# Performance work log

Measured on AMD Instinct MI355X. Metric: run time of the kernel, lower is better.

The kernel has to match this reference:

```python
import jax, jax.numpy as jnp
import numpy as np

B, N, M, D, F, H = 8, 512, 512, 512, 512, 8
D_H, F_H = D // H, F // H


def setup_inputs() -> dict:
    key = jax.random.key(0)
    ks = jax.random.split(key, 7)
    X = jax.random.normal(ks[0], (B, N, D), dtype=jnp.float32)
    V = jax.random.normal(ks[1], (B, M, F), dtype=jnp.float32)
    # learned parameters, init normal(0, 0.02) as in the torch module
    W_Q_1 = 0.02 * jax.random.normal(ks[2], (H, N, D_H, D_H), dtype=jnp.float32)
    W_Q_2 = 0.02 * jax.random.normal(ks[3], (H, N, M, D_H), dtype=jnp.float32)
    W_V = 0.02 * jax.random.normal(ks[4], (H, F_H, F_H), dtype=jnp.float32)
    O_w = 0.02 * jax.random.normal(ks[5], (F, F), dtype=jnp.float32)
    O_b = jnp.zeros((F,), dtype=jnp.float32)
    return {"X": X, "V": V, "W_Q_1": W_Q_1, "W_Q_2": W_Q_2,
            "W_V": W_V, "O_w": O_w, "O_b": O_b}


def reference(X, V, W_Q_1, W_Q_2, W_V, O_w, O_b):
    b, n, d = X.shape
    _, m, f = V.shape
    Xh = X.reshape(b, n, H, d // H)      # [B,N,H,D_H]
    Vh = V.reshape(b, m, H, f // H)      # [B,M,H,F_H]
    # 'hndd' repeats d within one operand -> diagonal of W_Q_1's last two dims
    # (faithful to torch.einsum semantics): per-position per-channel scale.
    Q_1 = jnp.einsum('bnhd,hndd->bhnd', Xh, W_Q_1)
    Q_1 = jax.nn.gelu(Q_1, approximate=False)  # torch nn.GELU default = exact erf
    Q_2 = jnp.einsum('bhnd,hnmd->bhnm', Q_1, W_Q_2)  # synthesized attention logits
    A = jax.nn.softmax(Q_2, axis=3)                  # softmax over M
    # 'hff' likewise takes the diagonal of W_V -> per-head channel scale fused
    # with the attention-weighted value aggregation.
    Y = jnp.einsum('bhnm,bmhf,hff->bnhf', A, Vh, W_V)
    Y = Y.reshape(b, n, f)
    return Y @ O_w.T + O_b
```

## Files before the change

### kernel.cpp

```cpp
#include <hip/hip_runtime.h>
#include <cstdint>

#define B_ 8
#define N_ 512
#define M_ 512
#define D_ 512
#define F_ 512
#define H_ 8
#define DH_ 64
#define FH_ 64

typedef __attribute__((ext_vector_type(8))) short bf16x8;
typedef __attribute__((ext_vector_type(4))) float f32x4;

__device__ __forceinline__ unsigned short f2bf(float x) {
    unsigned u = __float_as_uint(x);
    return (unsigned short)((u + 0x7fffu + ((u >> 16) & 1u)) >> 16);
}
__device__ __forceinline__ float bf2f(unsigned short b) {
    return __uint_as_float(((unsigned)b) << 16);
}

template <int CTRL>
__device__ __forceinline__ float dpp_add(float x) {
    int y = __builtin_amdgcn_update_dpp(0, __float_as_int(x), CTRL, 0xf, 0xf, true);
    return x + __int_as_float(y);
}

__global__ __launch_bounds__(256, 4) void syn_k_attn(const float* __restrict__ X,
                                                     const float* __restrict__ W1,
                                                     const float* __restrict__ W2,
                                                     float* __restrict__ A) {
    int hn = blockIdx.x;
    int h = hn >> 9, n = hn & 511;
    int t = threadIdx.x;
    int wave = t >> 6, lane = t & 63;
    __shared__ float q1s[8 * 68];
    __shared__ float logits[8 * 520];

    {
        int d = t & 63;
        int b0 = t >> 6;
        float w = W1[(size_t)hn * (DH_ * DH_) + d * (DH_ + 1)];
        #pragma unroll
        for (int i = 0; i < 2; ++i) {
            int bi = b0 + i * 4;
            float x = X[((size_t)(bi * N_ + n)) * D_ + h * DH_ + d];
            float v = x * w;
            q1s[bi * 68 + d] = 0.5f * v * (1.0f + erff(v * 0.70710678118654752440f));
        }
    }
    __syncthreads();

    int mr = lane >> 3, c = lane & 7;
    float4 qa[8], qb[8];
    #pragma unroll
    for (int b = 0; b < 8; ++b) {
        qa[b] = *(const float4*)&q1s[b * 68 + c * 8];
        qb[b] = *(const float4*)&q1s[b * 68 + c * 8 + 4];
    }

    const float* w2 = W2 + (size_t)hn * ((size_t)M_ * DH_);
    #pragma unroll 4
    for (int g = 0; g < 16; ++g) {
        int m = (wave + g * 4) * 8 + mr;
        const float* wr = w2 + (size_t)m * DH_ + c * 8;
        float4 wa = *(const float4*)wr;
        float4 wb = *(const float4*)(wr + 4);
        float acc[8];
        #pragma unroll
        for (int b = 0; b < 8; ++b) {
            float a0 = wa.x * qa[b].x + wa.y * qa[b].y + wa.z * qa[b].z + wa.w * qa[b].w
                     + wb.x * qb[b].x + wb.y * qb[b].y + wb.z * qb[b].z + wb.w * qb[b].w;
            a0 = dpp_add<0xB1>(a0);
            a0 = dpp_add<0x4E>(a0);
            a0 = dpp_add<0x124>(a0);
            acc[b] = a0;
        }
        float lo = c == 0 ? acc[0] : c == 1 ? acc[1] : c == 2 ? acc[2] : acc[3];
        float hi = c == 0 ? acc[4] : c == 1 ? acc[5] : c == 2 ? acc[6] : acc[7];
        if (c < 4) {
            logits[c * 520 + m] = lo;
            logits[(c + 4) * 520 + m] = hi;
        }
    }
    __syncthreads();

    for (int bb = wave; bb < 8; bb += 4) {
        const float* lrow = &logits[bb * 520 + lane * 8];
        float4 va = *(const float4*)lrow;
        float4 vb = *(const float4*)(lrow + 4);
        float v[8] = {va.x, va.y, va.z, va.w, vb.x, vb.y, vb.z, vb.w};
        float mx = v[0];
        #pragma unroll
        for (int i = 1; i < 8; ++i) mx = fmaxf(mx, v[i]);
        #pragma unroll
        for (int s = 1; s < 64; s <<= 1) mx = fmaxf(mx, __shfl_xor(mx, s));
        float e[8]; float sum = 0.f;
        #pragma unroll
        for (int i = 0; i < 8; ++i) { e[i] = expf(v[i] - mx); sum += e[i]; }
        #pragma unroll
        for (int s = 1; s < 64; s <<= 1) sum += __shfl_xor(sum, s);
        float inv = 1.0f / sum;
        float* outp = A + ((size_t)(bb * H_ + h) * N_ + n) * M_ + lane * 8;
        float4 o0 = make_float4(e[0] * inv, e[1] * inv, e[2] * inv, e[3] * inv);
        float4 o1 = make_float4(e[4] * inv, e[5] * inv, e[6] * inv, e[7] * inv);
        *(float4*)outp = o0;
        *(float4*)(outp + 4) = o1;
    }
}

__global__ __launch_bounds__(256) void syn_k_pv(const float* __restrict__ A,
                                                const float* __restrict__ V,
                                                const float* __restrict__ WV,
                                                unsigned short* __restrict__ Yhi,
                                                unsigned short* __restrict__ Ylo) {
    int bh = blockIdx.y;
    int b = bh >> 3, h = bh & 7;
    int n0 = blockIdx.x * 64;
    int t = threadIdx.x;
    int tx = t & 15, ty = t >> 4;
    __shared__ float Alds[64 * 64];
    __shared__ float Vlds[64 * 64];
    float acc[4][4] = {};
    const float* Abase = A + ((size_t)bh * N_ + n0) * M_;
    const float* Vbase = V + (size_t)b * ((size_t)M_ * F_) + h * FH_;
    int kk = tx * 4;
    for (int m0 = 0; m0 < M_; m0 += 64) {
        #pragma unroll
        for (int it = 0; it < 4; ++it) {
            int r = ty + it * 16;
            float4 a4 = *(const float4*)(Abase + (size_t)r * M_ + m0 + kk);
            int slot = ((r >> 2) ^ tx) & 15;
            float* p = &Alds[kk * 64 + slot * 4 + (r & 3)];
            p[0] = a4.x; p[64] = a4.y; p[128] = a4.z; p[192] = a4.w;
            float4 v4 = *(const float4*)(Vbase + (size_t)(m0 + r) * F_ + kk);
            *(float4*)&Vlds[r * 64 + kk] = v4;
        }
        __syncthreads();
        #pragma unroll 2
        for (int k4 = 0; k4 < 16; ++k4) {
            int sa = ((ty ^ k4) & 15) * 4;
            #pragma unroll
            for (int kj = 0; kj < 4; ++kj) {
                int k = k4 * 4 + kj;
                float4 a4 = *(const float4*)&Alds[k * 64 + sa];
                float4 v4 = *(const float4*)&Vlds[k * 64 + tx * 4];
                float ar[4] = {a4.x, a4.y, a4.z, a4.w};
                float vr[4] = {v4.x, v4.y, v4.z, v4.w};
                #pragma unroll
                for (int i = 0; i < 4; ++i)
                    #pragma unroll
                    for (int j = 0; j < 4; ++j)
                        acc[i][j] += ar[i] * vr[j];
            }
        }
        __syncthreads();
    }
    float s_[4];
    #pragma unroll
    for (int j = 0; j < 4; ++j)
        s_[j] = WV[(size_t)h * (FH_ * FH_) + (tx * 4 + j) * (FH_ + 1)];
    #pragma unroll
    for (int i = 0; i < 4; ++i) {
        int row = n0 + ty * 4 + i;
        float ys[4];
        #pragma unroll
        for (int j = 0; j < 4; ++j) ys[j] = acc[i][j] * s_[j];
        unsigned short hb[4], lb[4];
        #pragma unroll
        for (int j = 0; j < 4; ++j) {
            hb[j] = f2bf(ys[j]);
            lb[j] = f2bf(ys[j] - bf2f(hb[j]));
        }
        size_t base = ((size_t)(b * N_ + row)) * F_ + h * FH_ + tx * 4;
        uint2 hv, lv;
        hv.x = (unsigned)hb[0] | ((unsigned)hb[1] << 16);
        hv.y = (unsigned)hb[2] | ((unsigned)hb[3] << 16);
        lv.x = (unsigned)lb[0] | ((unsigned)lb[1] << 16);
        lv.y = (unsigned)lb[2] | ((unsigned)lb[3] << 16);
        *(uint2*)(Yhi + base) = hv;
        *(uint2*)(Ylo + base) = lv;
    }
}

__global__ __launch_bounds__(256) void syn_k_splitw(const float* __restrict__ Ow,
                                                    unsigned short* __restrict__ Whi,
                                                    unsigned short* __restrict__ Wlo) {
    int i = (blockIdx.x * 256 + threadIdx.x) * 4;
    float4 v = *(const float4*)(Ow + i);
    float vv[4] = {v.x, v.y, v.z, v.w};
    unsigned short hb[4], lb[4];
    #pragma unroll
    for (int j = 0; j < 4; ++j) {
        hb[j] = f2bf(vv[j]);
        lb[j] = f2bf(vv[j] - bf2f(hb[j]));
    }
    uint2 hv, lv;
    hv.x = (unsigned)hb[0] | ((unsigned)hb[1] << 16);
    hv.y = (unsigned)hb[2] | ((unsigned)hb[3] << 16);
    lv.x = (unsigned)lb[0] | ((unsigned)lb[1] << 16);
    lv.y = (unsigned)lb[2] | ((unsigned)lb[3] << 16);
    *(uint2*)(Whi + i) = hv;
    *(uint2*)(Wlo + i) = lv;
}

__global__ __launch_bounds__(256) void syn_k_out_mfma(const unsigned short* __restrict__ Yhi,
                                                      const unsigned short* __restrict__ Ylo,
                                                      const unsigned short* __restrict__ Whi,
                                                      const unsigned short* __restrict__ Wlo,
                                                      const float* __restrict__ Ob,
                                                      float* __restrict__ out) {
    int r0 = blockIdx.x * 64;
    int f0 = blockIdx.y * 64;
    int t = threadIdx.x;
    int lane = t & 63, wave = t >> 6;
    int wr = wave >> 1, wc = wave & 1;
    __shared__ __align__(16) unsigned short Al[64 * 64];
    __shared__ __align__(16) unsigned short Bl[64 * 64];
    f32x4 acc[2][2];
    #pragma unroll
    for (int i = 0; i < 2; ++i)
        #pragma unroll
        for (int j = 0; j < 2; ++j)
            acc[i][j] = (f32x4){0.f, 0.f, 0.f, 0.f};

    const unsigned short* Aseg[3] = {Yhi, Yhi, Ylo};
    const unsigned short* Bseg[3] = {Whi, Wlo, Whi};

    int srow = t >> 3, skg = t & 7;
    int sslot = skg ^ (srow & 7);
    unsigned aoff0 = srow * 64 + sslot * 8;
    unsigned aoff1 = (srow + 32) * 64 + sslot * 8;

    for (int seg = 0; seg < 3; ++seg) {
        const unsigned short* Ag0 = Aseg[seg] + (size_t)(r0 + srow) * 512 + skg * 8;
        const unsigned short* Ag1 = Aseg[seg] + (size_t)(r0 + srow + 32) * 512 + skg * 8;
        const unsigned short* Bg0 = Bseg[seg] + (size_t)(f0 + srow) * 512 + skg * 8;
        const unsigned short* Bg1 = Bseg[seg] + (size_t)(f0 + srow + 32) * 512 + skg * 8;
        #pragma unroll 1
        for (int kb = 0; kb < 512; kb += 64) {
            float4 a0 = *(const float4*)(Ag0 + kb);
            float4 a1 = *(const float4*)(Ag1 + kb);
            float4 b0 = *(const float4*)(Bg0 + kb);
            float4 b1 = *(const float4*)(Bg1 + kb);
            *(float4*)&Al[aoff0] = a0;
            *(float4*)&Al[aoff1] = a1;
            *(float4*)&Bl[aoff0] = b0;
            *(float4*)&Bl[aoff1] = b1;
            __syncthreads();
            #pragma unroll
            for (int m = 0; m < 2; ++m) {
                int kslot = (m * 4 + (lane >> 4)) ^ (lane & 7);
                bf16x8 af[2], bfr[2];
                #pragma unroll
                for (int q = 0; q < 2; ++q) {
                    int arow = wr * 32 + q * 16 + (lane & 15);
                    af[q] = *(const bf16x8*)&Al[arow * 64 + kslot * 8];
                    int brow = wc * 32 + q * 16 + (lane & 15);
                    bfr[q] = *(const bf16x8*)&Bl[brow * 64 + kslot * 8];
                }
                #pragma unroll
                for (int i = 0; i < 2; ++i)
                    #pragma unroll
                    for (int j = 0; j < 2; ++j)
                        acc[i][j] = __builtin_amdgcn_mfma_f32_16x16x32_bf16(
                            af[i], bfr[j], acc[i][j], 0, 0, 0);
            }
            __syncthreads();
        }
    }

    int crow = r0 + wr * 32 + (lane >> 4) * 4;
    int ccol = f0 + wc * 32 + (lane & 15);
    float ob0 = Ob[ccol], ob1 = Ob[ccol + 16];
    #pragma unroll
    for (int i = 0; i < 2; ++i)
        #pragma unroll
        for (int j = 0; j < 2; ++j) {
            float obv = (j == 0) ? ob0 : ob1;
            #pragma unroll
            for (int r = 0; r < 4; ++r) {
                int row = crow + i * 16 + r;
                out[(size_t)row * F_ + ccol + j * 16] = acc[i][j][r] + obv;
            }
        }
}

extern "C" void kernel_launch(void* const* d_in, const int* in_sizes, int n_in,
                              void* d_out, int out_size, void* d_ws, size_t ws_size,
                              hipStream_t stream) {
    const float* X  = (const float*)d_in[0];
    const float* V  = (const float*)d_in[1];
    const float* W1 = (const float*)d_in[2];
    const float* W2 = (const float*)d_in[3];
    const float* WV = (const float*)d_in[4];
    const float* Ow = (const float*)d_in[5];
    const float* Ob = (const float*)d_in[6];
    float* out = (float*)d_out;

    float* ws = (float*)d_ws;
    float* A = ws;
    unsigned short* Yhi = (unsigned short*)(A + (size_t)B_ * H_ * N_ * M_);
    unsigned short* Ylo = Yhi + (size_t)B_ * N_ * F_;
    unsigned short* Whi = Ylo + (size_t)B_ * N_ * F_;
    unsigned short* Wlo = Whi + (size_t)F_ * F_;

    syn_k_splitw<<<(F_ * F_) / (256 * 4), 256, 0, stream>>>(Ow, Whi, Wlo);
    syn_k_attn<<<H_ * N_, 256, 0, stream>>>(X, W1, W2, A);
    syn_k_pv<<<dim3(N_ / 64, B_ * H_), 256, 0, stream>>>(A, V, WV, Yhi, Ylo);
    syn_k_out_mfma<<<dim3((B_ * N_) / 64, F_ / 64), 256, 0, stream>>>(Yhi, Ylo, Whi, Wlo, Ob, out);
}
```

Measured before the change: 200.4 us.

## Move attention-value product to split-bf16 MFMA and fuse out-proj segments

Replaces the scalar FP32 A·V kernel with an MFMA kernel that splits A (on the fly) and V (via a new pre-transpose kernel into workspace) into bf16 hi/lo parts and runs three MFMAs per tile to emulate FP32 accuracy. The output projection is also restructured to load hi and lo tiles together in one pass instead of three sequential segments, which cuts global reloads of Yhi and Whi. The intent is to move the heavy A·V FLOPs off the vector ALUs onto matrix cores. In exchange it adds a V transpose/split launch, more LDS per block, and a small precision loss from dropping the lo·lo term.

```diff
diff --git a/kernel.cpp b/kernel.cpp
--- a/kernel.cpp
+++ b/kernel.cpp
@@ -12,6 +12,7 @@
 
 typedef __attribute__((ext_vector_type(8))) short bf16x8;
 typedef __attribute__((ext_vector_type(4))) float f32x4;
+typedef __attribute__((ext_vector_type(8))) unsigned short u16x8;
 
 __device__ __forceinline__ unsigned short f2bf(float x) {
     unsigned u = __float_as_uint(x);
@@ -110,80 +111,6 @@
     }
 }
 
-__global__ __launch_bounds__(256) void syn_k_pv(const float* __restrict__ A,
-                                                const float* __restrict__ V,
-                                                const float* __restrict__ WV,
-                                                unsigned short* __restrict__ Yhi,
-                                                unsigned short* __restrict__ Ylo) {
-    int bh = blockIdx.y;
-    int b = bh >> 3, h = bh & 7;
-    int n0 = blockIdx.x * 64;
-    int t = threadIdx.x;
-    int tx = t & 15, ty = t >> 4;
-    __shared__ float Alds[64 * 64];
-    __shared__ float Vlds[64 * 64];
-    float acc[4][4] = {};
-    const float* Abase = A + ((size_t)bh * N_ + n0) * M_;
-    const float* Vbase = V + (size_t)b * ((size_t)M_ * F_) + h * FH_;
-    int kk = tx * 4;
-    for (int m0 = 0; m0 < M_; m0 += 64) {
-        #pragma unroll
-        for (int it = 0; it < 4; ++it) {
-            int r = ty + it * 16;
-            float4 a4 = *(const float4*)(Abase + (size_t)r * M_ + m0 + kk);
-            int slot = ((r >> 2) ^ tx) & 15;
-            float* p = &Alds[kk * 64 + slot * 4 + (r & 3)];
-            p[0] = a4.x; p[64] = a4.y; p[128] = a4.z; p[192] = a4.w;
-            float4 v4 = *(const float4*)(Vbase + (size_t)(m0 + r) * F_ + kk);
-            *(float4*)&Vlds[r * 64 + kk] = v4;
-        }
-        __syncthreads();
-        #pragma unroll 2
-        for (int k4 = 0; k4 < 16; ++k4) {
-            int sa = ((ty ^ k4) & 15) * 4;
-            #pragma unroll
-            for (int kj = 0; kj < 4; ++kj) {
-                int k = k4 * 4 + kj;
-                float4 a4 = *(const float4*)&Alds[k * 64 + sa];
-                float4 v4 = *(const float4*)&Vlds[k * 64 + tx * 4];
-                float ar[4] = {a4.x, a4.y, a4.z, a4.w};
-                float vr[4] = {v4.x, v4.y, v4.z, v4.w};
-                #pragma unroll
-                for (int i = 0; i < 4; ++i)
-                    #pragma unroll
-                    for (int j = 0; j < 4; ++j)
-                        acc[i][j] += ar[i] * vr[j];
-            }
-        }
-        __syncthreads();
-    }
-    float s_[4];
-    #pragma unroll
-    for (int j = 0; j < 4; ++j)
-        s_[j] = WV[(size_t)h * (FH_ * FH_) + (tx * 4 + j) * (FH_ + 1)];
-    #pragma unroll
-    for (int i = 0; i < 4; ++i) {
-        int row = n0 + ty * 4 + i;
-        float ys[4];
-        #pragma unroll
-        for (int j = 0; j < 4; ++j) ys[j] = acc[i][j] * s_[j];
-        unsigned short hb[4], lb[4];
-        #pragma unroll
-        for (int j = 0; j < 4; ++j) {
-            hb[j] = f2bf(ys[j]);
-            lb[j] = f2bf(ys[j] - bf2f(hb[j]));
-        }
-        size_t base = ((size_t)(b * N_ + row)) * F_ + h * FH_ + tx * 4;
-        uint2 hv, lv;
-        hv.x = (unsigned)hb[0] | ((unsigned)hb[1] << 16);
-        hv.y = (unsigned)hb[2] | ((unsigned)hb[3] << 16);
-        lv.x = (unsigned)lb[0] | ((unsigned)lb[1] << 16);
-        lv.y = (unsigned)lb[2] | ((unsigned)lb[3] << 16);
-        *(uint2*)(Yhi + base) = hv;
-        *(uint2*)(Ylo + base) = lv;
-    }
-}
-
 __global__ __launch_bounds__(256) void syn_k_splitw(const float* __restrict__ Ow,
                                                     unsigned short* __restrict__ Whi,
                                                     unsigned short* __restrict__ Wlo) {
@@ -203,6 +130,133 @@
     lv.y = (unsigned)lb[2] | ((unsigned)lb[3] << 16);
     *(uint2*)(Whi + i) = hv;
     *(uint2*)(Wlo + i) = lv;
+}
+
+__global__ __launch_bounds__(256) void syn_k_splitv(const float* __restrict__ V,
+                                                    unsigned short* __restrict__ Vthi,
+                                                    unsigned short* __restrict__ Vtlo) {
+    int bh = blockIdx.x;
+    int b = bh >> 3, h = bh & 7;
+    int t = threadIdx.x;
+    __shared__ float lds[64 * 68];
+    for (int m0 = 0; m0 < M_; m0 += 64) {
+        int m = t >> 2, fo = (t & 3) * 16;
+        const float* src = V + ((size_t)(b * M_ + m0 + m)) * F_ + h * FH_ + fo;
+        #pragma unroll
+        for (int i = 0; i < 4; ++i)
+            *(float4*)&lds[m * 68 + fo + i * 4] = *(const float4*)(src + i * 4);
+        __syncthreads();
+        int f = t >> 2, mo = (t & 3) * 16;
+        unsigned short hb[16], lb[16];
+        #pragma unroll
+        for (int i = 0; i < 16; ++i) {
+            float x = lds[(mo + i) * 68 + f];
+            hb[i] = f2bf(x);
+            lb[i] = f2bf(x - bf2f(hb[i]));
+        }
+        size_t base = ((size_t)(bh * 64 + f)) * 512 + m0 + mo;
+        *(u16x8*)(Vthi + base) = *(u16x8*)hb;
+        *(u16x8*)(Vthi + base + 8) = *(u16x8*)&hb[8];
+        *(u16x8*)(Vtlo + base) = *(u16x8*)lb;
+        *(u16x8*)(Vtlo + base + 8) = *(u16x8*)&lb[8];
+        __syncthreads();
+    }
+}
+
+__global__ __launch_bounds__(256) void syn_k_pv_mfma(const float* __restrict__ A,
+                                                     const unsigned short* __restrict__ Vthi,
+                                                     const unsigned short* __restrict__ Vtlo,
+                                                     const float* __restrict__ WV,
+                                                     unsigned short* __restrict__ Yhi,
+                                                     unsigned short* __restrict__ Ylo) {
+    int bh = blockIdx.y;
+    int b = bh >> 3, h = bh & 7;
+    int n0 = blockIdx.x * 64;
+    int t = threadIdx.x;
+    int lane = t & 63, wave = t >> 6;
+    int wr = wave >> 1, wc = wave & 1;
+    __shared__ __align__(16) unsigned short Alh[64 * 64], All[64 * 64];
+    __shared__ __align__(16) unsigned short Blh[64 * 64], Bll[64 * 64];
+    f32x4 acc[2][2];
+    #pragma unroll
+    for (int i = 0; i < 2; ++i)
+        #pragma unroll
+        for (int j = 0; j < 2; ++j) acc[i][j] = (f32x4){0.f, 0.f, 0.f, 0.f};
+
+    int srow = t >> 3, skg = t & 7;
+    int sslot = skg ^ (srow & 7);
+    const float* Abase = A + ((size_t)bh * N_ + n0) * M_;
+    const unsigned short* Vhb = Vthi + ((size_t)bh * 64) * 512;
+    const unsigned short* Vlb = Vtlo + ((size_t)bh * 64) * 512;
+
+    #pragma unroll 1
+    for (int mb = 0; mb < 8; ++mb) {
+        int m0 = mb * 64;
+        #pragma unroll
+        for (int rr = 0; rr < 2; ++rr) {
+            int row = srow + rr * 32;
+            const float* ap = Abase + (size_t)row * M_ + m0 + skg * 8;
+            float4 x0 = *(const float4*)ap;
+            float4 x1 = *(const float4*)(ap + 4);
+            float xs[8] = {x0.x, x0.y, x0.z, x0.w, x1.x, x1.y, x1.z, x1.w};
+            unsigned short hb[8], lb[8];
+            #pragma unroll
+            for (int i = 0; i < 8; ++i) {
+                hb[i] = f2bf(xs[i]);
+                lb[i] = f2bf(xs[i] - bf2f(hb[i]));
+            }
+            *(u16x8*)&Alh[row * 64 + sslot * 8] = *(u16x8*)hb;
+            *(u16x8*)&All[row * 64 + sslot * 8] = *(u16x8*)lb;
+            *(u16x8*)&Blh[row * 64 + sslot * 8] =
+                *(const u16x8*)(Vhb + (size_t)row * 512 + m0 + skg * 8);
+            *(u16x8*)&Bll[row * 64 + sslot * 8] =
+                *(const u16x8*)(Vlb + (size_t)row * 512 + m0 + skg * 8);
+        }
+        __syncthreads();
+        #pragma unroll
+        for (int mg = 0; mg < 2; ++mg) {
+            int kslot = (mg * 4 + (lane >> 4)) ^ (lane & 7);
+            bf16x8 afh[2], afl[2], bfh[2], bfl[2];
+            #pragma unroll
+            for (int q = 0; q < 2; ++q) {
+                int arow = wr * 32 + q * 16 + (lane & 15);
+                afh[q] = *(const bf16x8*)&Alh[arow * 64 + kslot * 8];
+                afl[q] = *(const bf16x8*)&All[arow * 64 + kslot * 8];
+                int brow = wc * 32 + q * 16 + (lane & 15);
+                bfh[q] = *(const bf16x8*)&Blh[brow * 64 + kslot * 8];
+                bfl[q] = *(const bf16x8*)&Bll[brow * 64 + kslot * 8];
+            }
+            #pragma unroll
+            for (int i = 0; i < 2; ++i)
+                #pragma unroll
+                for (int j = 0; j < 2; ++j) {
+                    acc[i][j] = __builtin_amdgcn_mfma_f32_16x16x32_bf16(afh[i], bfh[j], acc[i][j], 0, 0, 0);
+                    acc[i][j] = __builtin_amdgcn_mfma_f32_16x16x32_bf16(afh[i], bfl[j], acc[i][j], 0, 0, 0);
+                    acc[i][j] = __builtin_amdgcn_mfma_f32_16x16x32_bf16(afl[i], bfh[j], acc[i][j], 0, 0, 0);
+                }
+        }
+        __syncthreads();
+    }
+
+    int crow = n0 + wr * 32 + (lane >> 4) * 4;
+    int ccol = wc * 32 + (lane & 15);
+    #pragma unroll
+    for (int j = 0; j < 2; ++j) {
+        int f = ccol + j * 16;
+        float s = WV[(size_t)h * (FH_ * FH_) + f * (FH_ + 1)];
+        #pragma unroll
+        for (int i = 0; i < 2; ++i)
+            #pragma unroll
+            for (int r = 0; r < 4; ++r) {
+                int row = crow + i * 16 + r;
+                float y = acc[i][j][r] * s;
+                unsigned short hb = f2bf(y);
+                unsigned short lb = f2bf(y - bf2f(hb));
+                size_t base = ((size_t)(b * N_ + row)) * F_ + h * FH_ + f;
+                Yhi[base] = hb;
+                Ylo[base] = lb;
+            }
+    }
 }
 
 __global__ __launch_bounds__(256) void syn_k_out_mfma(const unsigned short* __restrict__ Yhi,
@@ -216,59 +270,53 @@
     int t = threadIdx.x;
     int lane = t & 63, wave = t >> 6;
     int wr = wave >> 1, wc = wave & 1;
-    __shared__ __align__(16) unsigned short Al[64 * 64];
-    __shared__ __align__(16) unsigned short Bl[64 * 64];
+    __shared__ __align__(16) unsigned short Alh[64 * 64], All[64 * 64];
+    __shared__ __align__(16) unsigned short Blh[64 * 64], Bll[64 * 64];
     f32x4 acc[2][2];
     #pragma unroll
     for (int i = 0; i < 2; ++i)
         #pragma unroll
-        for (int j = 0; j < 2; ++j)
-            acc[i][j] = (f32x4){0.f, 0.f, 0.f, 0.f};
-
-    const unsigned short* Aseg[3] = {Yhi, Yhi, Ylo};
-    const unsigned short* Bseg[3] = {Whi, Wlo, Whi};
+        for (int j = 0; j < 2; ++j) acc[i][j] = (f32x4){0.f, 0.f, 0.f, 0.f};
 
     int srow = t >> 3, skg = t & 7;
     int sslot = skg ^ (srow & 7);
-    unsigned aoff0 = srow * 64 + sslot * 8;
-    unsigned aoff1 = (srow + 32) * 64 + sslot * 8;
-
-    for (int seg = 0; seg < 3; ++seg) {
-        const unsigned short* Ag0 = Aseg[seg] + (size_t)(r0 + srow) * 512 + skg * 8;
-        const unsigned short* Ag1 = Aseg[seg] + (size_t)(r0 + srow + 32) * 512 + skg * 8;
-        const unsigned short* Bg0 = Bseg[seg] + (size_t)(f0 + srow) * 512 + skg * 8;
-        const unsigned short* Bg1 = Bseg[seg] + (size_t)(f0 + srow + 32) * 512 + skg * 8;
-        #pragma unroll 1
-        for (int kb = 0; kb < 512; kb += 64) {
-            float4 a0 = *(const float4*)(Ag0 + kb);
-            float4 a1 = *(const float4*)(Ag1 + kb);
-            float4 b0 = *(const float4*)(Bg0 + kb);
-            float4 b1 = *(const float4*)(Bg1 + kb);
-            *(float4*)&Al[aoff0] = a0;
-            *(float4*)&Al[aoff1] = a1;
-            *(float4*)&Bl[aoff0] = b0;
-            *(float4*)&Bl[aoff1] = b1;
-            __syncthreads();
-            #pragma unroll
-            for (int m = 0; m < 2; ++m) {
-                int kslot = (m * 4 + (lane >> 4)) ^ (lane & 7);
-                bf16x8 af[2], bfr[2];
+
+    #pragma unroll 1
+    for (int kb = 0; kb < 512; kb += 64) {
+        #pragma unroll
+        for (int rr = 0; rr < 2; ++rr) {
+            int row = srow + rr * 32;
+            size_t ya = (size_t)(r0 + row) * 512 + kb + skg * 8;
+            size_t wa = (size_t)(f0 + row) * 512 + kb + skg * 8;
+            *(u16x8*)&Alh[row * 64 + sslot * 8] = *(const u16x8*)(Yhi + ya);
+            *(u16x8*)&All[row * 64 + sslot * 8] = *(const u16x8*)(Ylo + ya);
+            *(u16x8*)&Blh[row * 64 + sslot * 8] = *(const u16x8*)(Whi + wa);
+            *(u16x8*)&Bll[row * 64 + sslot * 8] = *(const u16x8*)(Wlo + wa);
+        }
+        __syncthreads();
+        #pragma unroll
+        for (int mg = 0; mg < 2; ++mg) {
+            int kslot = (mg * 4 + (lane >> 4)) ^ (lane & 7);
+            bf16x8 afh[2], afl[2], bfh[2], bfl[2];
+            #pragma unroll
+            for (int q = 0; q < 2; ++q) {
+                int arow = wr * 32 + q * 16 + (lane & 15);
+                afh[q] = *(const bf16x8*)&Alh[arow * 64 + kslot * 8];
+                afl[q] = *(const bf16x8*)&All[arow * 64 + kslot * 8];
+                int brow = wc * 32 + q * 16 + (lane & 15);
+                bfh[q] = *(const bf16x8*)&Blh[brow * 64 + kslot * 8];
+                bfl[q] = *(const bf16x8*)&Bll[brow * 64 + kslot * 8];
+            }
+            #pragma unroll
+            for (int i = 0; i < 2; ++i)
                 #pragma unroll
-                for (int q = 0; q < 2; ++q) {
-                    int arow = wr * 32 + q * 16 + (lane & 15);
-                    af[q] = *(const bf16x8*)&Al[arow * 64 + kslot * 8];
-                    int brow = wc * 32 + q * 16 + (lane & 15);
-                    bfr[q] = *(const bf16x8*)&Bl[brow * 64 + kslot * 8];
+                for (int j = 0; j < 2; ++j) {
+                    acc[i][j] = __builtin_amdgcn_mfma_f32_16x16x32_bf16(afh[i], bfh[j], acc[i][j], 0, 0, 0);
+                    acc[i][j] = __builtin_amdgcn_mfma_f32_16x16x32_bf16(afh[i], bfl[j], acc[i][j], 0, 0, 0);
+                    acc[i][j] = __builtin_amdgcn_mfma_f32_16x16x32_bf16(afl[i], bfh[j], acc[i][j], 0, 0, 0);
                 }
-                #pragma unroll
-                for (int i = 0; i < 2; ++i)
-                    #pragma unroll
-                    for (int j = 0; j < 2; ++j)
-                        acc[i][j] = __builtin_amdgcn_mfma_f32_16x16x32_bf16(
-                            af[i], bfr[j], acc[i][j], 0, 0, 0);
-            }
-            __syncthreads();
-        }
+        }
+        __syncthreads();
     }
 
     int crow = r0 + wr * 32 + (lane >> 4) * 4;
@@ -305,9 +353,12 @@
     unsigned short* Ylo = Yhi + (size_t)B_ * N_ * F_;
     unsigned short* Whi = Ylo + (size_t)B_ * N_ * F_;
     unsigned short* Wlo = Whi + (size_t)F_ * F_;
+    unsigned short* Vthi = Wlo + (size_t)F_ * F_;
+    unsigned short* Vtlo = Vthi + (size_t)B_ * H_ * FH_ * M_;
 
     syn_k_splitw<<<(F_ * F_) / (256 * 4), 256, 0, stream>>>(Ow, Whi, Wlo);
+    syn_k_splitv<<<B_ * H_, 256, 0, stream>>>(V, Vthi, Vtlo);
     syn_k_attn<<<H_ * N_, 256, 0, stream>>>(X, W1, W2, A);
-    syn_k_pv<<<dim3(N_ / 64, B_ * H_), 256, 0, stream>>>(A, V, WV, Yhi, Ylo);
+    syn_k_pv_mfma<<<dim3(N_ / 64, B_ * H_), 256, 0, stream>>>(A, Vthi, Vtlo, WV, Yhi, Ylo);
     syn_k_out_mfma<<<dim3((B_ * N_) / 64, F_ / 64), 256, 0, stream>>>(Yhi, Ylo, Whi, Wlo, Ob, out);
 }
```

Measured after the change: 190.7 us. 1.05x faster.
